# Performance work log

Hardware: AMD Instinct MI355X
Metric: run time of the kernel (lower is better)

## Reference

```python
import jax, jax.numpy as jnp
import numpy as np

B, T, F, H = 16384, 36, 18, 128  # batch, seq_len(=size_seq), dim_seq_in, rnn_out


def setup_inputs() -> dict:
    key = jax.random.key(0)
    ks = jax.random.split(key, 12)
    s = 0.05
    return {
        "seqs": jax.random.normal(ks[0], (B, T, F), jnp.float32),
        "mask": jnp.ones((B, T, 1), jnp.float32),
        # InputAttention params (torch Linear: y = x @ W.T + b)
        "Wh": jax.random.normal(ks[1], (T, H), jnp.float32) * s,   # linearHidden
        "bh": jax.random.normal(ks[2], (T,), jnp.float32) * s,
        "Ws": jax.random.normal(ks[3], (T, T), jnp.float32) * s,   # linearSignals
        "bs": jax.random.normal(ks[4], (T,), jnp.float32) * s,
        "Wo": jax.random.normal(ks[5], (1, T), jnp.float32) * s,   # linearOut
        "bo": jax.random.normal(ks[6], (1,), jnp.float32) * s,
        # GRU params (torch layout: gates ordered r, z, n)
        "W_ih": jax.random.normal(ks[7], (3 * H, F), jnp.float32) * s,
        "W_hh": jax.random.normal(ks[8], (3 * H, H), jnp.float32) * s,
        "b_ih": jax.random.normal(ks[9], (3 * H,), jnp.float32) * s,
        "b_hh": jax.random.normal(ks[10], (3 * H,), jnp.float32) * s,
    }


def reference(seqs, mask, Wh, bh, Ws, bs, Wo, bo, W_ih, W_hh, b_ih, b_hh):
    # seqs: [B,T,F]; mask: [B,T,1]
    Hv = W_hh.shape[1]
    # Attention signal projection is computed from the ORIGINAL seqs and is
    # constant across timesteps: signal_k = seqs.transpose(1,2) -> [B,F,T]
    signal_k = jnp.swapaxes(seqs, 1, 2)
    lin_signal = signal_k @ Ws.T + bs  # [B,F,T]

    def step(h, x_t):
        # h: [B,H] previous GRU hidden; x_t: [B,F] raw input at step t
        lin_h = h @ Wh.T + bh                              # [B,T]
        tan = jnp.tanh(lin_h[:, None, :] + lin_signal)     # [B,F,T]
        e = tan @ Wo[0] + bo[0]                            # [B,F]
        att = jax.nn.softmax(e, axis=1)                    # softmax over features
        x = att * x_t                                      # scaled input
        # GRU cell (torch gate order r,z,n)
        gi = x @ W_ih.T + b_ih                             # [B,3H]
        gh = h @ W_hh.T + b_hh
        r = jax.nn.sigmoid(gi[:, :Hv] + gh[:, :Hv])
        z = jax.nn.sigmoid(gi[:, Hv:2 * Hv] + gh[:, Hv:2 * Hv])
        n = jnp.tanh(gi[:, 2 * Hv:] + r * gh[:, 2 * Hv:])
        h_new = (1.0 - z) * n + z * h
        return h_new, h_new

    h0 = jnp.zeros((seqs.shape[0], Hv), seqs.dtype)
    _, hs = jax.lax.scan(step, h0, jnp.swapaxes(seqs, 0, 1))  # hs: [T,B,H]
    hidden = jnp.swapaxes(hs, 0, 1)                            # [B,T,H]
    return (hidden * mask).sum(axis=1)                         # [B,H]
```

## Files before the change

kernel.cpp:

```cpp
#include <hip/hip_runtime.h>
#include <hip/hip_bf16.h>
#include <hip/hip_fp8.h>

#define TT 36
#define FF 18
#define HH 128
#define BB 16
#define BLOCK 512
#define SIGP 36

typedef __attribute__((ext_vector_type(4))) float f32x4;

#define L2E  1.4426950408889634f
#define L2E2 2.8853900817779268f

#if __has_builtin(__builtin_amdgcn_rcpf)
static __device__ __forceinline__ float frcp(float x) { return __builtin_amdgcn_rcpf(x); }
#else
static __device__ __forceinline__ float frcp(float x) { return 1.f / x; }
#endif
#if __has_builtin(__builtin_amdgcn_exp2f)
static __device__ __forceinline__ float fexp2(float x) { return __builtin_amdgcn_exp2f(x); }
#else
static __device__ __forceinline__ float fexp2(float x) { return __expf(x * 0.69314718056f); }
#endif

#if __has_builtin(__builtin_amdgcn_cvt_pk_fp8_f32)
static __device__ __forceinline__ unsigned char f2fp8(float f) {
    int v = __builtin_amdgcn_cvt_pk_fp8_f32(f, 0.f, 0, false);
    return (unsigned char)(v & 0xff);
}
#else
static __device__ __forceinline__ unsigned char f2fp8(float f) {
    __hip_fp8_e4m3 q(f);
    return *(unsigned char*)&q;
}
#endif

static __device__ __forceinline__ f32x4 mfma_f8(long a, long b, f32x4 c) {
    return __builtin_amdgcn_mfma_f32_16x16x32_fp8_fp8(a, b, c, 0, 0, 0);
}

union F8x8 { unsigned char b[8]; long l; };

static __device__ __forceinline__ unsigned hxoff(int c, int bb) {
    return (unsigned)((c * BB + (bb ^ c)) << 3);
}

__global__ __launch_bounds__(BLOCK, 4) void enc_att_gru(
    const float* __restrict__ seqs, const float* __restrict__ mask,
    const float* __restrict__ Wh,   const float* __restrict__ bh,
    const float* __restrict__ Ws,   const float* __restrict__ bs,
    const float* __restrict__ Wo,   const float* __restrict__ bo,
    const float* __restrict__ W_ih, const float* __restrict__ W_hh,
    const float* __restrict__ b_ih, const float* __restrict__ b_hh,
    float* __restrict__ out)
{
    __shared__ __align__(16) float es_lds[BB * FF * SIGP];
    __shared__ float Ws2_lds[TT * TT];
    __shared__ float bs2_lds[TT];
    __shared__ __align__(16) float wo2_lds[TT];
    __shared__ __align__(16) float el_lds[BB][SIGP];
    __shared__ __align__(16) unsigned char h_lds[16 * BB * 8];
    __shared__ __align__(16) unsigned char x_lds[4 * BB * 8];
    __shared__ float mask_lds[BB][TT];
    __shared__ __align__(16) long whf_lds[4 * 3 * 64];

    const int tid  = threadIdx.x;
    const int wave = tid >> 6;
    const int lane = tid & 63;
    const int l15  = lane & 15;
    const int l4   = lane >> 4;
    const int bbase = blockIdx.x * BB;
    const int bb2 = tid >> 5;
    const int f2  = tid & 31;
    const int fsafe = (f2 < FF) ? f2 : (FF - 1);

    for (int idx = tid; idx < TT * TT; idx += BLOCK) {
        int t = idx / TT, tp = idx - t * TT;
        Ws2_lds[tp * TT + t] = L2E2 * Ws[idx];
    }
    if (tid < TT) { bs2_lds[tid] = L2E2 * bs[tid]; wo2_lds[tid] = -2.f * Wo[tid]; }
    for (int idx = tid; idx < BB * TT; idx += BLOCK) {
        int bb = idx / TT, t = idx - bb * TT;
        mask_lds[bb][t] = mask[(size_t)(bbase + bb) * TT + t];
    }
    for (int idx = tid; idx < 16 * BB * 2; idx += BLOCK) ((int*)h_lds)[idx] = 0;
    for (int idx = tid; idx < 4 * BB * 2; idx += BLOCK) ((int*)x_lds)[idx] = 0;
    for (int e = tid; e < 4 * 3 * 64; e += BLOCK) {
        int kt = e / 192;
        int w  = (e / 64) % 3;
        int l  = e & 63;
        int tcolw = w * 16 + (l & 15);
        int kb = kt * 32 + ((l >> 4) & 3) * 8;
        F8x8 u;
#pragma unroll
        for (int jj = 0; jj < 8; ++jj)
            u.b[jj] = (tcolw < TT) ? f2fp8(Wh[(size_t)tcolw * HH + kb + jj]) : (unsigned char)0;
        whf_lds[e] = u.l;
    }
    __syncthreads();

    if (f2 < FF) {
        const size_t sb = (size_t)(bbase + bb2) * (TT * FF) + f2;
        float* srow = &es_lds[(bb2 * FF + f2) * SIGP];
        for (int c = 0; c < 3; ++c) {
            float acc[12];
#pragma unroll
            for (int j = 0; j < 12; ++j) acc[j] = bs2_lds[c * 12 + j];
            for (int tp = 0; tp < TT; ++tp) {
                float s = seqs[sb + (size_t)tp * FF];
#pragma unroll
                for (int j = 0; j < 12; ++j)
                    acc[j] = fmaf(s, Ws2_lds[tp * TT + c * 12 + j], acc[j]);
            }
#pragma unroll
            for (int j = 0; j < 12; ++j) srow[c * 12 + j] = fexp2(acc[j]);
        }
    }

    long whh[3][4];
    for (int g = 0; g < 3; ++g)
        for (int kt = 0; kt < 4; ++kt) {
            const int o = g * HH + 16 * wave + l15;
            F8x8 u;
#pragma unroll
            for (int jj = 0; jj < 8; ++jj) {
                int k = kt * 32 + l4 * 8 + jj;
                u.b[jj] = f2fp8(W_hh[(size_t)o * HH + k]);
            }
            whh[g][kt] = u.l;
        }
    long wih[3];
    for (int g = 0; g < 3; ++g) {
        const int o = g * HH + 16 * wave + l15;
        F8x8 u;
#pragma unroll
        for (int jj = 0; jj < 8; ++jj) {
            int f = l4 * 8 + jj;
            u.b[jj] = (f < FF) ? f2fp8(W_ih[(size_t)o * FF + f]) : (unsigned char)0;
        }
        wih[g] = u.l;
    }
    const int tcol = 16 * wave + l15;
    const int junit = 16 * wave + l15;
    const float brz_r = b_ih[junit] + b_hh[junit];
    const float brz_z = b_ih[HH + junit] + b_hh[HH + junit];
    const float bn_i  = b_ih[2 * HH + junit];
    const float bn_h  = b_hh[2 * HH + junit];
    const float bh_reg = (wave < 3 && tcol < TT) ? bh[tcol] : 0.f;
    float c0 = bo[0];
    for (int tp = 0; tp < TT; ++tp) c0 += Wo[tp];

    float seq_cur = seqs[(size_t)(bbase + bb2) * (TT * FF) + fsafe];

    float h_prev[4]  = {0.f, 0.f, 0.f, 0.f};
    float out_acc[4] = {0.f, 0.f, 0.f, 0.f};

    __syncthreads();

    for (int t = 0; t < TT; ++t) {
        long ha[4];
#pragma unroll
        for (int kt = 0; kt < 4; ++kt)
            ha[kt] = *(const long*)(h_lds + hxoff(kt * 4 + l4, l15));
        if (wave < 3) {
            f32x4 a = {0.f, 0.f, 0.f, 0.f};
#pragma unroll
            for (int kt = 0; kt < 4; ++kt)
                a = mfma_f8(ha[kt], whf_lds[kt * 192 + wave * 64 + lane], a);
            if (tcol < TT) {
#pragma unroll
                for (int r = 0; r < 4; ++r)
                    el_lds[l4 * 4 + r][tcol] = fexp2((a[r] + bh_reg) * L2E2);
            }
        }
        f32x4 acc_r = {0.f,0.f,0.f,0.f}, acc_z = {0.f,0.f,0.f,0.f}, acc_n = {0.f,0.f,0.f,0.f};
#pragma unroll
        for (int kt = 0; kt < 4; ++kt) {
            acc_r = mfma_f8(ha[kt], whh[0][kt], acc_r);
            acc_z = mfma_f8(ha[kt], whh[1][kt], acc_z);
            acc_n = mfma_f8(ha[kt], whh[2][kt], acc_n);
        }
        __syncthreads();

        {
            const float* srow = &es_lds[(bb2 * FF + fsafe) * SIGP];
            const float* lrow = &el_lds[bb2][0];
            float a0 = c0, a1 = 0.f, a2 = 0.f, a3 = 0.f;
#pragma unroll
            for (int g = 0; g < 9; ++g) {
                f32x4 sv = *(const f32x4*)(srow + g * 4);
                f32x4 lv = *(const f32x4*)(lrow + g * 4);
                f32x4 wv = *(const f32x4*)(&wo2_lds[g * 4]);
                a0 = fmaf(wv[0], frcp(fmaf(sv[0], lv[0], 1.f)), a0);
                a1 = fmaf(wv[1], frcp(fmaf(sv[1], lv[1], 1.f)), a1);
                a2 = fmaf(wv[2], frcp(fmaf(sv[2], lv[2], 1.f)), a2);
                a3 = fmaf(wv[3], frcp(fmaf(sv[3], lv[3], 1.f)), a3);
            }
            float eacc = (a0 + a1) + (a2 + a3);
            float p = (f2 < FF) ? fexp2(L2E * eacc) : 0.f;
            float s = p;
#pragma unroll
            for (int d = 1; d <= 16; d <<= 1) s += __shfl_xor(s, d);
            if (f2 < FF) {
                x_lds[hxoff(f2 >> 3, bb2) + (f2 & 7)] = f2fp8(p * frcp(s) * seq_cur);
                if (t + 1 < TT)
                    seq_cur = seqs[(size_t)(bbase + bb2) * (TT * FF) + (size_t)(t + 1) * FF + f2];
            }
        }
        __syncthreads();

        long xa = *(const long*)(x_lds + hxoff(l4, l15));
        acc_r = mfma_f8(xa, wih[0], acc_r);
        acc_z = mfma_f8(xa, wih[1], acc_z);
        f32x4 zero4 = {0.f, 0.f, 0.f, 0.f};
        f32x4 acc_gi = mfma_f8(xa, wih[2], zero4);
#pragma unroll
        for (int r = 0; r < 4; ++r) {
            int bb = l4 * 4 + r;
            float rg = frcp(1.f + fexp2(-L2E * (acc_r[r] + brz_r)));
            float zg = frcp(1.f + fexp2(-L2E * (acc_z[r] + brz_z)));
            float gin = acc_gi[r] + bn_i + rg * (acc_n[r] + bn_h);
            float ng = 1.f - 2.f * frcp(1.f + fexp2(L2E2 * gin));
            float hn = fmaf(zg, h_prev[r] - ng, ng);
            h_prev[r] = hn;
            out_acc[r] = fmaf(hn, mask_lds[bb][t], out_acc[r]);
            h_lds[hxoff(junit >> 3, bb) + (junit & 7)] = f2fp8(hn);
        }
        __syncthreads();
    }

#pragma unroll
    for (int r = 0; r < 4; ++r) {
        int bb = l4 * 4 + r;
        out[(size_t)(bbase + bb) * HH + junit] = out_acc[r];
    }
}

extern "C" void kernel_launch(void* const* d_in, const int* in_sizes, int n_in,
                              void* d_out, int out_size, void* d_ws, size_t ws_size,
                              hipStream_t stream) {
    const float* seqs = (const float*)d_in[0];
    const float* mask = (const float*)d_in[1];
    const float* Wh   = (const float*)d_in[2];
    const float* bh   = (const float*)d_in[3];
    const float* Ws   = (const float*)d_in[4];
    const float* bs   = (const float*)d_in[5];
    const float* Wo   = (const float*)d_in[6];
    const float* bo   = (const float*)d_in[7];
    const float* W_ih = (const float*)d_in[8];
    const float* W_hh = (const float*)d_in[9];
    const float* b_ih = (const float*)d_in[10];
    const float* b_hh = (const float*)d_in[11];
    float* out = (float*)d_out;

    const int Btot = in_sizes[0] / (TT * FF);
    const int grid = Btot / BB;
    enc_att_gru<<<grid, BLOCK, 0, stream>>>(seqs, mask, Wh, bh, Ws, bs, Wo, bo,
                                            W_ih, W_hh, b_ih, b_hh, out);
}
```

Measured before the change: 262.2 us.

## Process 32 batch rows per block with bf16 attention signal cache

Doubles the batch tile per block from 16 to 32 rows. Each wave now runs two 16-row MFMA tiles against the same register-resident W_hh/W_ih fragments, and each attention thread handles two batch rows. The exponentiated signal table is stored as bf16 so the doubled tile fits in the same LDS footprint. Mask is transposed so a step's values load as one vector. The aim is to amortise weight setup, per-step barriers and per-block prologue over twice the rows and halve the block count. In exchange, the hidden-state MFMAs now run after the attention phase rather than overlapping it, and bf16 rounding of the signal adds precision risk.

After: 535.1 us. +104.1%, slower.

```diff
diff --git a/kernel.cpp b/kernel.cpp
--- a/kernel.cpp
+++ b/kernel.cpp
@@ -5,15 +5,26 @@
 #define TT 36
 #define FF 18
 #define HH 128
-#define BB 16
+#define BB 32
 #define BLOCK 512
-#define SIGP 36
+#define ESP 36
+#define ELP 36
 
 typedef __attribute__((ext_vector_type(4))) float f32x4;
+typedef __attribute__((ext_vector_type(4))) unsigned short u16x4;
 
 #define L2E  1.4426950408889634f
 #define L2E2 2.8853900817779268f
 
+static __device__ __forceinline__ float bf2f(unsigned short u) {
+    unsigned int x = ((unsigned int)u) << 16;
+    return __builtin_bit_cast(float, x);
+}
+static __device__ __forceinline__ unsigned short f2bf(float f) {
+    unsigned int x = __builtin_bit_cast(unsigned int, f);
+    unsigned int r = (x + 0x7fffu + ((x >> 16) & 1u)) >> 16;
+    return (unsigned short)r;
+}
 #if __has_builtin(__builtin_amdgcn_rcpf)
 static __device__ __forceinline__ float frcp(float x) { return __builtin_amdgcn_rcpf(x); }
 #else
@@ -56,14 +67,14 @@
     const float* __restrict__ b_ih, const float* __restrict__ b_hh,
     float* __restrict__ out)
 {
-    __shared__ __align__(16) float es_lds[BB * FF * SIGP];
+    __shared__ __align__(16) unsigned short es_lds[BB * FF * ESP];
     __shared__ float Ws2_lds[TT * TT];
     __shared__ float bs2_lds[TT];
     __shared__ __align__(16) float wo2_lds[TT];
-    __shared__ __align__(16) float el_lds[BB][SIGP];
+    __shared__ __align__(16) float el_lds[BB][ELP];
     __shared__ __align__(16) unsigned char h_lds[16 * BB * 8];
     __shared__ __align__(16) unsigned char x_lds[4 * BB * 8];
-    __shared__ float mask_lds[BB][TT];
+    __shared__ __align__(16) float mask_t[TT][BB];
     __shared__ __align__(16) long whf_lds[4 * 3 * 64];
 
     const int tid  = threadIdx.x;
@@ -72,7 +83,8 @@
     const int l15  = lane & 15;
     const int l4   = lane >> 4;
     const int bbase = blockIdx.x * BB;
-    const int bb2 = tid >> 5;
+    const int bb2a = tid >> 5;
+    const int bb2b = bb2a + 16;
     const int f2  = tid & 31;
     const int fsafe = (f2 < FF) ? f2 : (FF - 1);
 
@@ -83,7 +95,7 @@
     if (tid < TT) { bs2_lds[tid] = L2E2 * bs[tid]; wo2_lds[tid] = -2.f * Wo[tid]; }
     for (int idx = tid; idx < BB * TT; idx += BLOCK) {
         int bb = idx / TT, t = idx - bb * TT;
-        mask_lds[bb][t] = mask[(size_t)(bbase + bb) * TT + t];
+        mask_t[t][bb] = mask[(size_t)(bbase + bb) * TT + t];
     }
     for (int idx = tid; idx < 16 * BB * 2; idx += BLOCK) ((int*)h_lds)[idx] = 0;
     for (int idx = tid; idx < 4 * BB * 2; idx += BLOCK) ((int*)x_lds)[idx] = 0;
@@ -101,9 +113,11 @@
     }
     __syncthreads();
 
-    if (f2 < FF) {
-        const size_t sb = (size_t)(bbase + bb2) * (TT * FF) + f2;
-        float* srow = &es_lds[(bb2 * FF + f2) * SIGP];
+    for (int task = tid; task < BB * FF; task += BLOCK) {
+        const int bb = task / FF;
+        const int f  = task - bb * FF;
+        const size_t sb = (size_t)(bbase + bb) * (TT * FF) + f;
+        unsigned short* srow = &es_lds[task * ESP];
         for (int c = 0; c < 3; ++c) {
             float acc[12];
 #pragma unroll
@@ -115,7 +129,7 @@
                     acc[j] = fmaf(s, Ws2_lds[tp * TT + c * 12 + j], acc[j]);
             }
 #pragma unroll
-            for (int j = 0; j < 12; ++j) srow[c * 12 + j] = fexp2(acc[j]);
+            for (int j = 0; j < 12; ++j) srow[c * 12 + j] = f2bf(fexp2(acc[j]));
         }
     }
 
@@ -142,100 +156,131 @@
         }
         wih[g] = u.l;
     }
-    const int tcol = 16 * wave + l15;
+    const int wgrp = (wave < 4) ? wave : (wave - 4);
+    const bool linh_wave = (wgrp < 3);
+    const int lrt  = (wave < 4) ? 0 : 1;
+    const int tcol = wgrp * 16 + l15;
     const int junit = 16 * wave + l15;
     const float brz_r = b_ih[junit] + b_hh[junit];
     const float brz_z = b_ih[HH + junit] + b_hh[HH + junit];
     const float bn_i  = b_ih[2 * HH + junit];
     const float bn_h  = b_hh[2 * HH + junit];
-    const float bh_reg = (wave < 3 && tcol < TT) ? bh[tcol] : 0.f;
+    const float bh_reg = (linh_wave && tcol < TT) ? bh[tcol] : 0.f;
     float c0 = bo[0];
     for (int tp = 0; tp < TT; ++tp) c0 += Wo[tp];
 
-    float seq_cur = seqs[(size_t)(bbase + bb2) * (TT * FF) + fsafe];
-
-    float h_prev[4]  = {0.f, 0.f, 0.f, 0.f};
-    float out_acc[4] = {0.f, 0.f, 0.f, 0.f};
+    float seq_curA = seqs[(size_t)(bbase + bb2a) * (TT * FF) + fsafe];
+    float seq_curB = seqs[(size_t)(bbase + bb2b) * (TT * FF) + fsafe];
+
+    float h_prev[2][4]  = {{0.f,0.f,0.f,0.f},{0.f,0.f,0.f,0.f}};
+    float out_acc[2][4] = {{0.f,0.f,0.f,0.f},{0.f,0.f,0.f,0.f}};
 
     __syncthreads();
 
     for (int t = 0; t < TT; ++t) {
-        long ha[4];
-#pragma unroll
-        for (int kt = 0; kt < 4; ++kt)
-            ha[kt] = *(const long*)(h_lds + hxoff(kt * 4 + l4, l15));
-        if (wave < 3) {
+        if (linh_wave) {
+            long ha0[4];
+#pragma unroll
+            for (int kt = 0; kt < 4; ++kt)
+                ha0[kt] = *(const long*)(h_lds + hxoff(kt * 4 + l4, lrt * 16 + l15));
             f32x4 a = {0.f, 0.f, 0.f, 0.f};
 #pragma unroll
             for (int kt = 0; kt < 4; ++kt)
-                a = mfma_f8(ha[kt], whf_lds[kt * 192 + wave * 64 + lane], a);
+                a = mfma_f8(ha0[kt], whf_lds[kt * 192 + wgrp * 64 + lane], a);
             if (tcol < TT) {
 #pragma unroll
                 for (int r = 0; r < 4; ++r)
-                    el_lds[l4 * 4 + r][tcol] = fexp2((a[r] + bh_reg) * L2E2);
-            }
-        }
-        f32x4 acc_r = {0.f,0.f,0.f,0.f}, acc_z = {0.f,0.f,0.f,0.f}, acc_n = {0.f,0.f,0.f,0.f};
-#pragma unroll
-        for (int kt = 0; kt < 4; ++kt) {
-            acc_r = mfma_f8(ha[kt], whh[0][kt], acc_r);
-            acc_z = mfma_f8(ha[kt], whh[1][kt], acc_z);
-            acc_n = mfma_f8(ha[kt], whh[2][kt], acc_n);
+                    el_lds[lrt * 16 + l4 * 4 + r][tcol] = fexp2((a[r] + bh_reg) * L2E2);
+            }
         }
         __syncthreads();
 
         {
-            const float* srow = &es_lds[(bb2 * FF + fsafe) * SIGP];
-            const float* lrow = &el_lds[bb2][0];
+            const unsigned short* srA = &es_lds[(bb2a * FF + fsafe) * ESP];
+            const unsigned short* srB = &es_lds[(bb2b * FF + fsafe) * ESP];
+            const float* lrA = &el_lds[bb2a][0];
+            const float* lrB = &el_lds[bb2b][0];
             float a0 = c0, a1 = 0.f, a2 = 0.f, a3 = 0.f;
+            float b0 = c0, b1 = 0.f, b2 = 0.f, b3 = 0.f;
 #pragma unroll
             for (int g = 0; g < 9; ++g) {
-                f32x4 sv = *(const f32x4*)(srow + g * 4);
-                f32x4 lv = *(const f32x4*)(lrow + g * 4);
+                u16x4 ua = *(const u16x4*)(srA + g * 4);
+                u16x4 ub = *(const u16x4*)(srB + g * 4);
+                f32x4 la = *(const f32x4*)(lrA + g * 4);
+                f32x4 lb = *(const f32x4*)(lrB + g * 4);
                 f32x4 wv = *(const f32x4*)(&wo2_lds[g * 4]);
-                a0 = fmaf(wv[0], frcp(fmaf(sv[0], lv[0], 1.f)), a0);
-                a1 = fmaf(wv[1], frcp(fmaf(sv[1], lv[1], 1.f)), a1);
-                a2 = fmaf(wv[2], frcp(fmaf(sv[2], lv[2], 1.f)), a2);
-                a3 = fmaf(wv[3], frcp(fmaf(sv[3], lv[3], 1.f)), a3);
-            }
-            float eacc = (a0 + a1) + (a2 + a3);
-            float p = (f2 < FF) ? fexp2(L2E * eacc) : 0.f;
-            float s = p;
-#pragma unroll
-            for (int d = 1; d <= 16; d <<= 1) s += __shfl_xor(s, d);
+                a0 = fmaf(wv[0], frcp(fmaf(bf2f(ua[0]), la[0], 1.f)), a0);
+                a1 = fmaf(wv[1], frcp(fmaf(bf2f(ua[1]), la[1], 1.f)), a1);
+                a2 = fmaf(wv[2], frcp(fmaf(bf2f(ua[2]), la[2], 1.f)), a2);
+                a3 = fmaf(wv[3], frcp(fmaf(bf2f(ua[3]), la[3], 1.f)), a3);
+                b0 = fmaf(wv[0], frcp(fmaf(bf2f(ub[0]), lb[0], 1.f)), b0);
+                b1 = fmaf(wv[1], frcp(fmaf(bf2f(ub[1]), lb[1], 1.f)), b1);
+                b2 = fmaf(wv[2], frcp(fmaf(bf2f(ub[2]), lb[2], 1.f)), b2);
+                b3 = fmaf(wv[3], frcp(fmaf(bf2f(ub[3]), lb[3], 1.f)), b3);
+            }
+            float eA = (a0 + a1) + (a2 + a3);
+            float eB = (b0 + b1) + (b2 + b3);
+            float pA = (f2 < FF) ? fexp2(L2E * eA) : 0.f;
+            float pB = (f2 < FF) ? fexp2(L2E * eB) : 0.f;
+            float sA = pA, sB = pB;
+#pragma unroll
+            for (int d = 1; d <= 16; d <<= 1) {
+                sA += __shfl_xor(sA, d);
+                sB += __shfl_xor(sB, d);
+            }
             if (f2 < FF) {
-                x_lds[hxoff(f2 >> 3, bb2) + (f2 & 7)] = f2fp8(p * frcp(s) * seq_cur);
-                if (t + 1 < TT)
-                    seq_cur = seqs[(size_t)(bbase + bb2) * (TT * FF) + (size_t)(t + 1) * FF + f2];
+                x_lds[hxoff(f2 >> 3, bb2a) + (f2 & 7)] = f2fp8(pA * frcp(sA) * seq_curA);
+                x_lds[hxoff(f2 >> 3, bb2b) + (f2 & 7)] = f2fp8(pB * frcp(sB) * seq_curB);
+                if (t + 1 < TT) {
+                    seq_curA = seqs[(size_t)(bbase + bb2a) * (TT * FF) + (size_t)(t + 1) * FF + f2];
+                    seq_curB = seqs[(size_t)(bbase + bb2b) * (TT * FF) + (size_t)(t + 1) * FF + f2];
+                }
             }
         }
         __syncthreads();
 
-        long xa = *(const long*)(x_lds + hxoff(l4, l15));
-        acc_r = mfma_f8(xa, wih[0], acc_r);
-        acc_z = mfma_f8(xa, wih[1], acc_z);
-        f32x4 zero4 = {0.f, 0.f, 0.f, 0.f};
-        f32x4 acc_gi = mfma_f8(xa, wih[2], zero4);
+#pragma unroll
+        for (int rt = 0; rt < 2; ++rt) {
+            long ha[4];
+#pragma unroll
+            for (int kt = 0; kt < 4; ++kt)
+                ha[kt] = *(const long*)(h_lds + hxoff(kt * 4 + l4, rt * 16 + l15));
+            f32x4 ar = {0.f,0.f,0.f,0.f}, az = {0.f,0.f,0.f,0.f}, an = {0.f,0.f,0.f,0.f};
+#pragma unroll
+            for (int kt = 0; kt < 4; ++kt) {
+                ar = mfma_f8(ha[kt], whh[0][kt], ar);
+                az = mfma_f8(ha[kt], whh[1][kt], az);
+                an = mfma_f8(ha[kt], whh[2][kt], an);
+            }
+            long xa = *(const long*)(x_lds + hxoff(l4, rt * 16 + l15));
+            ar = mfma_f8(xa, wih[0], ar);
+            az = mfma_f8(xa, wih[1], az);
+            f32x4 zero4 = {0.f, 0.f, 0.f, 0.f};
+            f32x4 agi = mfma_f8(xa, wih[2], zero4);
+            f32x4 mv = *(const f32x4*)(&mask_t[t][rt * 16 + l4 * 4]);
+#pragma unroll
+            for (int r = 0; r < 4; ++r) {
+                int bb = rt * 16 + l4 * 4 + r;
+                float rg = frcp(1.f + fexp2(-L2E * (ar[r] + brz_r)));
+                float zg = frcp(1.f + fexp2(-L2E * (az[r] + brz_z)));
+                float gin = agi[r] + bn_i + rg * (an[r] + bn_h);
+                float ng = fmaf(-2.f, frcp(1.f + fexp2(L2E2 * gin)), 1.f);
+                float hn = fmaf(zg, h_prev[rt][r] - ng, ng);
+                h_prev[rt][r] = hn;
+                out_acc[rt][r] = fmaf(hn, mv[r], out_acc[rt][r]);
+                h_lds[hxoff(junit >> 3, bb) + (junit & 7)] = f2fp8(hn);
+            }
+        }
+        __syncthreads();
+    }
+
+#pragma unroll
+    for (int rt = 0; rt < 2; ++rt)
 #pragma unroll
         for (int r = 0; r < 4; ++r) {
-            int bb = l4 * 4 + r;
-            float rg = frcp(1.f + fexp2(-L2E * (acc_r[r] + brz_r)));
-            float zg = frcp(1.f + fexp2(-L2E * (acc_z[r] + brz_z)));
-            float gin = acc_gi[r] + bn_i + rg * (acc_n[r] + bn_h);
-            float ng = 1.f - 2.f * frcp(1.f + fexp2(L2E2 * gin));
-            float hn = fmaf(zg, h_prev[r] - ng, ng);
-            h_prev[r] = hn;
-            out_acc[r] = fmaf(hn, mask_lds[bb][t], out_acc[r]);
-            h_lds[hxoff(junit >> 3, bb) + (junit & 7)] = f2fp8(hn);
-        }
-        __syncthreads();
-    }
-
-#pragma unroll
-    for (int r = 0; r < 4; ++r) {
-        int bb = l4 * 4 + r;
-        out[(size_t)(bbase + bb) * HH + junit] = out_acc[r];
-    }
+            int bb = rt * 16 + l4 * 4 + r;
+            out[(size_t)(bbase + bb) * HH + junit] = out_acc[rt][r];
+        }
 }
 
 extern "C" void kernel_launch(void* const* d_in, const int* in_sizes, int n_in,
```
